# Performance work log

Measured on AMD Instinct MI355X. Metric: run time of the kernel, lower is better.

The kernel has to match this reference:

```python
import jax, jax.numpy as jnp
import numpy as np

B, V, FN, C = 8, 50000, 100000, 64


def setup_inputs() -> dict:
    key = jax.random.key(0)
    keys = iter(jax.random.split(key, 16))
    inp = {}
    inp["centers"] = jax.random.normal(next(keys), (B, 3, FN), jnp.float32)
    inp["verts"] = jax.random.normal(next(keys), (B, V, 3), jnp.float32)
    inp["faces"] = jax.random.randint(next(keys), (B, FN, 3), 0, V)

    def bn(p):
        inp[p + "g"] = jnp.ones((C,), jnp.float32)
        inp[p + "bt"] = jnp.zeros((C,), jnp.float32)
        inp[p + "m"] = jnp.zeros((C,), jnp.float32)
        inp[p + "v"] = jnp.ones((C,), jnp.float32)

    inp["cw1"] = jax.random.normal(next(keys), (C, 3), jnp.float32) * 0.1
    inp["cb1"] = jnp.zeros((C,), jnp.float32); bn("c1")
    inp["cw2"] = jax.random.normal(next(keys), (C, C), jnp.float32) * 0.1
    inp["cb2"] = jnp.zeros((C,), jnp.float32); bn("c2")
    inp["vw1"] = jax.random.normal(next(keys), (C, 6), jnp.float32) * 0.1
    inp["vb1"] = jnp.zeros((C,), jnp.float32); bn("v1")
    inp["vw2"] = jax.random.normal(next(keys), (C, C), jnp.float32) * 0.1
    inp["vb2"] = jnp.zeros((C,), jnp.float32); bn("v2")
    inp["sw"] = jax.random.normal(next(keys), (C, 2 * C), jnp.float32) * 0.1
    inp["sb"] = jnp.zeros((C,), jnp.float32); bn("s1")
    return inp


def _cbr(x, w, b, g, bt, m, v, eps=1e-5):
    # 1x1 Conv1d == pointwise GEMM over channel dim, then eval-mode BN, then ReLU
    y = jnp.einsum('bcf,oc->bof', x, w) + b[:, None]
    y = (y - m[:, None]) * (g[:, None] / jnp.sqrt(v[:, None] + eps)) + bt[:, None]
    return jax.nn.relu(y)


def _forward(faces, centers, verts,
             cw1, cb1, c1g, c1bt, c1m, c1v, cw2, cb2, c2g, c2bt, c2m, c2v,
             vw1, vb1, v1g, v1bt, v1m, v1v, vw2, vb2, v2g, v2bt, v2m, v2v,
             sw, sb, s1g, s1bt, s1m, s1v):
    Bb, Fn, _ = faces.shape
    # gather 3 corner vertices per face: [B, 3F, 3] -> [B, 9, F] (v0xyz, v1xyz, v2xyz)
    idx = faces.reshape(Bb, Fn * 3)
    corners = jnp.take_along_axis(verts, idx[:, :, None], axis=1)
    c9 = corners.reshape(Bb, Fn, 9).transpose(0, 2, 1)

    def vmlp(x):
        return _cbr(_cbr(x, vw1, vb1, v1g, v1bt, v1m, v1v), vw2, vb2, v2g, v2bt, v2m, v2v)

    vfeat = (vmlp(c9[:, :6])
             + vmlp(c9[:, 3:9])
             + vmlp(jnp.concatenate([c9[:, 6:9], c9[:, :3]], axis=1))) / 3.0
    cfeat = _cbr(_cbr(centers, cw1, cb1, c1g, c1bt, c1m, c1v), cw2, cb2, c2g, c2bt, c2m, c2v)
    return _cbr(jnp.concatenate([cfeat, vfeat], axis=1), sw, sb, s1g, s1bt, s1m, s1v)


def reference(centers, verts, faces,
              cw1, cb1, c1g, c1bt, c1m, c1v, cw2, cb2, c2g, c2bt, c2m, c2v,
              vw1, vb1, v1g, v1bt, v1m, v1v, vw2, vb2, v2g, v2bt, v2m, v2v,
              sw, sb, s1g, s1bt, s1m, s1v):
    return _forward(faces, centers, verts,
                    cw1, cb1, c1g, c1bt, c1m, c1v, cw2, cb2, c2g, c2bt, c2m, c2v,
                    vw1, vb1, v1g, v1bt, v1m, v1v, vw2, vb2, v2g, v2bt, v2m, v2v,
                    sw, sb, s1g, s1bt, s1m, s1v)
```

## Files before the change

kernel.cpp:

```cpp
#include <hip/hip_runtime.h>
#include <cstddef>
#include <cstdint>

#define FN_ 100000
#define V_  50000
#define B_  8
#define WPB   8
#define NBLK  3125

#define WS_SHS 49152

typedef _Float16 f16;
typedef f16   f16x8 __attribute__((ext_vector_type(8)));
typedef float f32x4 __attribute__((ext_vector_type(4)));

struct Ptrs { const void* p[33]; };

union Pk8 { f16 h[8]; uint4 u; };
union FragU { uint32_t u[4]; f16x8 v; };

__device__ __forceinline__ uint32_t pack2(float a, float b) {
  return __builtin_bit_cast(uint32_t, __builtin_amdgcn_cvt_pkrtz(a, b));
}
__device__ __forceinline__ uint32_t pack_relu2(float a, float b) {
  uint32_t r, x = pack2(a, b);
  asm("v_pk_max_f16 %0, %1, 0" : "=v"(r) : "v"(x));
  return r;
}

__global__ __launch_bounds__(1024) void sd_prep(Ptrs in, f16* __restrict__ wsW,
                                                float* __restrict__ shsG)
{
  const float* __restrict__ cw1 = (const float*)in.p[3];
  const float* __restrict__ cb1 = (const float*)in.p[4];
  const float* __restrict__ c1g = (const float*)in.p[5];
  const float* __restrict__ c1bt= (const float*)in.p[6];
  const float* __restrict__ c1m = (const float*)in.p[7];
  const float* __restrict__ c1v = (const float*)in.p[8];
  const float* __restrict__ cw2 = (const float*)in.p[9];
  const float* __restrict__ cb2 = (const float*)in.p[10];
  const float* __restrict__ c2g = (const float*)in.p[11];
  const float* __restrict__ c2bt= (const float*)in.p[12];
  const float* __restrict__ c2m = (const float*)in.p[13];
  const float* __restrict__ c2v = (const float*)in.p[14];
  const float* __restrict__ vw1 = (const float*)in.p[15];
  const float* __restrict__ vb1 = (const float*)in.p[16];
  const float* __restrict__ v1g = (const float*)in.p[17];
  const float* __restrict__ v1bt= (const float*)in.p[18];
  const float* __restrict__ v1m = (const float*)in.p[19];
  const float* __restrict__ v1v = (const float*)in.p[20];
  const float* __restrict__ vw2 = (const float*)in.p[21];
  const float* __restrict__ vb2 = (const float*)in.p[22];
  const float* __restrict__ v2g = (const float*)in.p[23];
  const float* __restrict__ v2bt= (const float*)in.p[24];
  const float* __restrict__ v2m = (const float*)in.p[25];
  const float* __restrict__ v2v = (const float*)in.p[26];
  const float* __restrict__ sw  = (const float*)in.p[27];
  const float* __restrict__ sb  = (const float*)in.p[28];
  const float* __restrict__ s1g = (const float*)in.p[29];
  const float* __restrict__ s1bt= (const float*)in.p[30];
  const float* __restrict__ s1m = (const float*)in.p[31];
  const float* __restrict__ s1v = (const float*)in.p[32];

  __shared__ float scsL[448];
  __shared__ float shfL[256];
  const int tid = threadIdx.x;

  if (tid < 448) {
    const float *g, *v, *bb, *m, *bt; int o; float mul = 1.f;
    if (tid < 64)       { o = tid;      g=c1g; v=c1v; bb=cb1; m=c1m; bt=c1bt; }
    else if (tid < 256) { o = tid & 63; g=v1g; v=v1v; bb=vb1; m=v1m; bt=v1bt; }
    else if (tid < 320) { o = tid-256;  g=c2g; v=c2v; bb=cb2; m=c2m; bt=c2bt; }
    else if (tid < 384) { o = tid-320;  g=v2g; v=v2v; bb=vb2; m=v2m; bt=v2bt; mul = 1.f/3.f; }
    else                { o = tid-384;  g=s1g; v=s1v; bb=sb;  m=s1m; bt=s1bt; }
    float s = g[o] * rsqrtf(v[o] + 1e-5f);
    float sh = ((bb[o] - m[o]) * s + bt[o]) * mul;
    scsL[tid] = s * mul;
    shsG[tid] = sh;
    if (tid < 256) shfL[tid] = sh;
  }
  __syncthreads();

  for (int u = tid; u < 3072; u += 1024) {
    const int t = u >> 6, l = u & 63, r15 = l & 15, g4 = l >> 4;
    Pk8 pk;
    if (t < 16) {
      const int wm = t >> 2, tr = t & 3, row = 64*wm + 16*tr + r15;
#pragma unroll
      for (int j = 0; j < 8; ++j) {
        const int k = 8*g4 + j; float val = 0.f;
        if (wm == 0) { if (k >= 9 && k < 12) val = cw1[row*3 + (k-9)]; }
        else if (k < 9) {
          const int e = wm - 1, o = row - 64*wm, c = (k - 3*e + 9) % 9;
          if (c < 6) val = vw1[o*6 + c];
        }
        pk.h[j] = (k == 12) ? (f16)shfL[row] : (f16)(val * scsL[row]);
      }
    } else if (t < 24) {
      const int tt = t-16, rt = tt >> 1, s = tt & 1, row = 16*rt + r15;
#pragma unroll
      for (int j = 0; j < 8; ++j) { const int k = 32*s + 8*g4 + j;
        pk.h[j] = (f16)(cw2[row*64 + k] * scsL[256+row]); }
    } else if (t < 32) {
      const int tt = t-24, rt = tt >> 1, s = tt & 1, row = 16*rt + r15;
#pragma unroll
      for (int j = 0; j < 8; ++j) { const int k = 32*s + 8*g4 + j;
        pk.h[j] = (f16)(vw2[row*64 + k] * scsL[320+row]); }
    } else {
      const int tt = t-32, rt = tt >> 2, s = tt & 3, row = 16*rt + r15;
#pragma unroll
      for (int j = 0; j < 8; ++j) { const int k = 32*s + 8*g4 + j;
        pk.h[j] = (f16)(sw[row*128 + k] * scsL[384+row]); }
    }
    *(uint4*)(wsW + (size_t)t*512 + l*8) = pk.u;
  }
}

__global__ __launch_bounds__(512, 4) void sd_main(const int* __restrict__ faces,
    const float* __restrict__ verts, const float* __restrict__ centers,
    const f16* __restrict__ wsW, const float* __restrict__ shsG,
    float* __restrict__ out)
{
  __shared__ f16  Wl[32 * 512];
  __shared__ f16  Ab[WPB][32 * 64];
  __shared__ float shsL[192];

  const int tid  = threadIdx.x;
  const int lane = tid & 63;
  const int r15  = lane & 15;
  const int g4   = lane >> 4;
  const int w    = __builtin_amdgcn_readfirstlane(tid >> 6);
  const int sw   = (r15 & 7) << 3;

  {
    const uint4* src = (const uint4*)wsW;
    uint4* dst = (uint4*)Wl;
#pragma unroll
    for (int i = 0; i < 4; ++i) dst[tid + i*512] = src[tid + i*512];
  }
  if (tid < 192) shsL[tid] = shsG[256 + tid];

  const int wt = blockIdx.x * WPB + w;
  const int by = wt / 3125;
  const int f0 = (wt - by * 3125) * 32;

  FragU xf[2];
#pragma unroll
  for (int c = 0; c < 2; ++c) {
    float vals[8] = {0.f,0.f,0.f,0.f,0.f,0.f,0.f,0.f};
    const int f = f0 + 16*c + r15;
    if (g4 == 0) {
      const size_t fb3 = ((size_t)by*FN_ + f)*3;
      const int i0 = faces[fb3], i1 = faces[fb3+1], i2 = faces[fb3+2];
      const float* q0 = verts + ((size_t)by*V_ + (size_t)i0)*3;
      const float* q1 = verts + ((size_t)by*V_ + (size_t)i1)*3;
      const float* q2 = verts + ((size_t)by*V_ + (size_t)i2)*3;
      vals[0]=q0[0]; vals[1]=q0[1]; vals[2]=q0[2];
      vals[3]=q1[0]; vals[4]=q1[1]; vals[5]=q1[2];
      vals[6]=q2[0]; vals[7]=q2[1];
    } else if (g4 == 1) {
      const size_t fb3 = ((size_t)by*FN_ + f)*3;
      const int i2 = faces[fb3+2];
      const float* q2 = verts + ((size_t)by*V_ + (size_t)i2)*3;
      vals[0]=q2[2];
      vals[1]=centers[((size_t)by*3+0)*FN_ + f];
      vals[2]=centers[((size_t)by*3+1)*FN_ + f];
      vals[3]=centers[((size_t)by*3+2)*FN_ + f];
      vals[4]=1.0f;
    }
#pragma unroll
    for (int m = 0; m < 4; ++m) xf[c].u[m] = pack2(vals[2*m], vals[2*m+1]);
  }
  __syncthreads();

  f16* ab = &Ab[w][0];

  float    vf[4][2][4];
  uint32_t cfp[4][2][2];

#pragma unroll
  for (int br = 0; br < 4; ++br) {
    f32x4 acc1[4][2];
#pragma unroll
    for (int t4 = 0; t4 < 4; ++t4) {
      const f16x8 a = *(const f16x8*)&Wl[(4*br + t4)*512 + lane*8];
#pragma unroll
      for (int c = 0; c < 2; ++c) {
        f32x4 z = {0.f,0.f,0.f,0.f};
        acc1[t4][c] = __builtin_amdgcn_mfma_f32_16x16x32_f16(a, xf[c].v, z, 0,0,0);
      }
    }
#pragma unroll
    for (int t4 = 0; t4 < 4; ++t4)
#pragma unroll
      for (int c = 0; c < 2; ++c) {
        uint2 pw;
        pw.x = pack_relu2(acc1[t4][c][0], acc1[t4][c][1]);
        pw.y = pack_relu2(acc1[t4][c][2], acc1[t4][c][3]);
        *(uint2*)&ab[(16*c + r15)*64 + ((16*t4 + 4*g4) ^ sw)] = pw;
      }

    f16x8 b2[2][2];
#pragma unroll
    for (int c = 0; c < 2; ++c)
#pragma unroll
      for (int s = 0; s < 2; ++s)
        b2[c][s] = *(const f16x8*)&ab[(16*c + r15)*64 + ((32*s + 8*g4) ^ sw)];

    const int wb = br ? 24 : 16;
    const int shb = br ? 64 : 0;
#pragma unroll
    for (int rt = 0; rt < 4; ++rt) {
      const f16x8 a0 = *(const f16x8*)&Wl[(wb + 2*rt    )*512 + lane*8];
      const f16x8 a1 = *(const f16x8*)&Wl[(wb + 2*rt + 1)*512 + lane*8];
      const f32x4 shv = *(const f32x4*)&shsL[shb + rt*16 + 4*g4];
#pragma unroll
      for (int c = 0; c < 2; ++c) {
        f32x4 acc = __builtin_amdgcn_mfma_f32_16x16x32_f16(a0, b2[c][0], shv, 0,0,0);
        acc = __builtin_amdgcn_mfma_f32_16x16x32_f16(a1, b2[c][1], acc, 0,0,0);
        if (br == 0) {
          cfp[rt][c][0] = pack_relu2(acc[0], acc[1]);
          cfp[rt][c][1] = pack_relu2(acc[2], acc[3]);
        } else if (br == 1) {
#pragma unroll
          for (int j = 0; j < 4; ++j) vf[rt][c][j] = fmaxf(acc[j], 0.f);
        } else {
#pragma unroll
          for (int j = 0; j < 4; ++j) vf[rt][c][j] += fmaxf(acc[j], 0.f);
        }
      }
    }
  }

  f32x4 acc3[4][2];
#pragma unroll
  for (int rt = 0; rt < 4; ++rt) {
    const f32x4 shv = *(const f32x4*)&shsL[128 + rt*16 + 4*g4];
    acc3[rt][0] = shv; acc3[rt][1] = shv;
  }

#pragma unroll
  for (int half = 0; half < 2; ++half) {
#pragma unroll
    for (int rt = 0; rt < 4; ++rt)
#pragma unroll
      for (int c = 0; c < 2; ++c) {
        uint2 pw;
        if (half == 0) { pw.x = cfp[rt][c][0]; pw.y = cfp[rt][c][1]; }
        else { pw.x = pack2(vf[rt][c][0], vf[rt][c][1]);
               pw.y = pack2(vf[rt][c][2], vf[rt][c][3]); }
        *(uint2*)&ab[(16*c + r15)*64 + ((16*rt + 4*g4) ^ sw)] = pw;
      }
#pragma unroll
    for (int s = 0; s < 2; ++s) {
      f16x8 b[2];
#pragma unroll
      for (int c = 0; c < 2; ++c)
        b[c] = *(const f16x8*)&ab[(16*c + r15)*64 + ((32*s + 8*g4) ^ sw)];
#pragma unroll
      for (int rt = 0; rt < 4; ++rt) {
        const f16x8 aS = *(const f16x8*)(wsW + (size_t)(32 + 4*rt + 2*half + s)*512 + lane*8);
        acc3[rt][0] = __builtin_amdgcn_mfma_f32_16x16x32_f16(aS, b[0], acc3[rt][0], 0,0,0);
        acc3[rt][1] = __builtin_amdgcn_mfma_f32_16x16x32_f16(aS, b[1], acc3[rt][1], 0,0,0);
      }
    }
  }

#pragma unroll
  for (int rt = 0; rt < 4; ++rt)
#pragma unroll
    for (int c = 0; c < 2; ++c) {
      const size_t base = ((size_t)(by*64 + rt*16 + 4*g4))*FN_ + (size_t)(f0 + 16*c + r15);
#pragma unroll
      for (int j = 0; j < 4; ++j)
        out[base + (size_t)j*FN_] = fmaxf(acc3[rt][c][j], 0.f);
    }
}

extern "C" void kernel_launch(void* const* d_in, const int* in_sizes, int n_in,
                              void* d_out, int out_size, void* d_ws, size_t ws_size,
                              hipStream_t stream) {
  (void)in_sizes; (void)n_in; (void)out_size; (void)ws_size;
  Ptrs p;
  for (int i = 0; i < 33; ++i) p.p[i] = d_in[i];
  f16*   wsW  = (f16*)d_ws;
  float* shsG = (float*)((char*)d_ws + WS_SHS);
  hipLaunchKernelGGL(sd_prep, dim3(1), dim3(1024), 0, stream, p, wsW, shsG);
  hipLaunchKernelGGL(sd_main, dim3(NBLK), dim3(512), 0, stream,
                     (const int*)d_in[2], (const float*)d_in[1], (const float*)d_in[0],
                     wsW, shsG, (float*)d_out);
}
```

Baseline: 89.05 us.

## Use 16x16x16 MFMA for first layer and keep weights in registers

The K=13 first-layer GEMM now uses the 16x16x16 f16 MFMA with 4-half fragments instead of a zero-padded K=32 MFMA. The packed weight workspace is rearranged so that layer-1 weights and the vertex second-layer weights are loaded straight from global memory into registers, and shared memory keeps only the center second-layer weights. This shrinks the per-block LDS weight copy from 32 KB to 8 KB and halves layer-1 MFMA work. The cost is higher register pressure, which could reduce occupancy or cause spills.

Measured after the change: 117.0 us. 1.31x slower.

```diff
diff --git a/kernel.cpp b/kernel.cpp
--- a/kernel.cpp
+++ b/kernel.cpp
@@ -8,16 +8,18 @@
 #define WPB   8
 #define NBLK  3125
 
-#define WS_SHS 49152
+#define WS_SHS_OFF 40960
 
 typedef _Float16 f16;
+typedef f16   f16x4 __attribute__((ext_vector_type(4)));
 typedef f16   f16x8 __attribute__((ext_vector_type(8)));
 typedef float f32x4 __attribute__((ext_vector_type(4)));
 
 struct Ptrs { const void* p[33]; };
 
+union Pk4h { f16 h[4]; uint2 u; };
 union Pk8 { f16 h[8]; uint4 u; };
-union FragU { uint32_t u[4]; f16x8 v; };
+union FragU4 { uint32_t u[2]; f16x4 v; };
 
 __device__ __forceinline__ uint32_t pack2(float a, float b) {
   return __builtin_bit_cast(uint32_t, __builtin_amdgcn_cvt_pkrtz(a, b));
@@ -81,38 +83,44 @@
   }
   __syncthreads();
 
-  for (int u = tid; u < 3072; u += 1024) {
-    const int t = u >> 6, l = u & 63, r15 = l & 15, g4 = l >> 4;
+  {
+    const int t = tid >> 6, l = tid & 63, r15l = l & 15, g4l = l >> 4;
+    const int row = 16*t + r15l;
+    const int wm = t >> 2;
+    Pk4h pk;
+#pragma unroll
+    for (int j = 0; j < 4; ++j) {
+      const int k = 4*g4l + j; float val = 0.f;
+      if (wm == 0) { if (k >= 9 && k < 12) val = cw1[row*3 + (k-9)]; }
+      else if (k < 9) {
+        const int e = wm - 1, o = row - 64*wm, c = (k - 3*e + 9) % 9;
+        if (c < 6) val = vw1[o*6 + c];
+      }
+      pk.h[j] = (k == 12) ? (f16)shfL[row] : (f16)(val * scsL[row]);
+    }
+    *(uint2*)((char*)wsW + t*512 + l*8) = pk.u;
+  }
+
+  for (int u = tid; u < 2560; u += 1024) {
+    const int t = u >> 6, l = u & 63, r15l = l & 15, g4l = l >> 4;
     Pk8 pk;
-    if (t < 16) {
-      const int wm = t >> 2, tr = t & 3, row = 64*wm + 16*tr + r15;
-#pragma unroll
-      for (int j = 0; j < 8; ++j) {
-        const int k = 8*g4 + j; float val = 0.f;
-        if (wm == 0) { if (k >= 9 && k < 12) val = cw1[row*3 + (k-9)]; }
-        else if (k < 9) {
-          const int e = wm - 1, o = row - 64*wm, c = (k - 3*e + 9) % 9;
-          if (c < 6) val = vw1[o*6 + c];
-        }
-        pk.h[j] = (k == 12) ? (f16)shfL[row] : (f16)(val * scsL[row]);
-      }
-    } else if (t < 24) {
-      const int tt = t-16, rt = tt >> 1, s = tt & 1, row = 16*rt + r15;
-#pragma unroll
-      for (int j = 0; j < 8; ++j) { const int k = 32*s + 8*g4 + j;
+    if (t < 8) {
+      const int rt = t >> 1, s = t & 1, row = 16*rt + r15l;
+#pragma unroll
+      for (int j = 0; j < 8; ++j) { const int k = 32*s + 8*g4l + j;
         pk.h[j] = (f16)(cw2[row*64 + k] * scsL[256+row]); }
-    } else if (t < 32) {
-      const int tt = t-24, rt = tt >> 1, s = tt & 1, row = 16*rt + r15;
-#pragma unroll
-      for (int j = 0; j < 8; ++j) { const int k = 32*s + 8*g4 + j;
+    } else if (t < 16) {
+      const int tt = t-8, rt = tt >> 1, s = tt & 1, row = 16*rt + r15l;
+#pragma unroll
+      for (int j = 0; j < 8; ++j) { const int k = 32*s + 8*g4l + j;
         pk.h[j] = (f16)(vw2[row*64 + k] * scsL[320+row]); }
     } else {
-      const int tt = t-32, rt = tt >> 2, s = tt & 3, row = 16*rt + r15;
-#pragma unroll
-      for (int j = 0; j < 8; ++j) { const int k = 32*s + 8*g4 + j;
+      const int tt = t-16, rt = tt >> 2, s4 = tt & 3, row = 16*rt + r15l;
+#pragma unroll
+      for (int j = 0; j < 8; ++j) { const int k = 32*s4 + 8*g4l + j;
         pk.h[j] = (f16)(sw[row*128 + k] * scsL[384+row]); }
     }
-    *(uint4*)(wsW + (size_t)t*512 + l*8) = pk.u;
+    *(uint4*)((char*)wsW + 8192 + t*1024 + l*16) = pk.u;
   }
 }
 
@@ -121,7 +129,7 @@
     const f16* __restrict__ wsW, const float* __restrict__ shsG,
     float* __restrict__ out)
 {
-  __shared__ f16  Wl[32 * 512];
+  __shared__ f16  Wl[8 * 512];
   __shared__ f16  Ab[WPB][32 * 64];
   __shared__ float shsL[192];
 
@@ -133,10 +141,8 @@
   const int sw   = (r15 & 7) << 3;
 
   {
-    const uint4* src = (const uint4*)wsW;
-    uint4* dst = (uint4*)Wl;
-#pragma unroll
-    for (int i = 0; i < 4; ++i) dst[tid + i*512] = src[tid + i*512];
+    const uint4* src = (const uint4*)((const char*)wsW + 8192);
+    ((uint4*)Wl)[tid] = src[tid];
   }
   if (tid < 192) shsL[tid] = shsG[256 + tid];
 
@@ -144,33 +150,45 @@
   const int by = wt / 3125;
   const int f0 = (wt - by * 3125) * 32;
 
-  FragU xf[2];
+  FragU4 xf[2];
 #pragma unroll
   for (int c = 0; c < 2; ++c) {
-    float vals[8] = {0.f,0.f,0.f,0.f,0.f,0.f,0.f,0.f};
+    float vals[4] = {0.f, 0.f, 0.f, 0.f};
     const int f = f0 + 16*c + r15;
+    const size_t fb3 = ((size_t)by*FN_ + f)*3;
     if (g4 == 0) {
-      const size_t fb3 = ((size_t)by*FN_ + f)*3;
-      const int i0 = faces[fb3], i1 = faces[fb3+1], i2 = faces[fb3+2];
+      const int i0 = faces[fb3], i1 = faces[fb3+1];
       const float* q0 = verts + ((size_t)by*V_ + (size_t)i0)*3;
       const float* q1 = verts + ((size_t)by*V_ + (size_t)i1)*3;
+      vals[0]=q0[0]; vals[1]=q0[1]; vals[2]=q0[2]; vals[3]=q1[0];
+    } else if (g4 == 1) {
+      const int i1 = faces[fb3+1], i2 = faces[fb3+2];
+      const float* q1 = verts + ((size_t)by*V_ + (size_t)i1)*3;
       const float* q2 = verts + ((size_t)by*V_ + (size_t)i2)*3;
-      vals[0]=q0[0]; vals[1]=q0[1]; vals[2]=q0[2];
-      vals[3]=q1[0]; vals[4]=q1[1]; vals[5]=q1[2];
-      vals[6]=q2[0]; vals[7]=q2[1];
-    } else if (g4 == 1) {
-      const size_t fb3 = ((size_t)by*FN_ + f)*3;
+      vals[0]=q1[1]; vals[1]=q1[2]; vals[2]=q2[0]; vals[3]=q2[1];
+    } else if (g4 == 2) {
       const int i2 = faces[fb3+2];
       const float* q2 = verts + ((size_t)by*V_ + (size_t)i2)*3;
       vals[0]=q2[2];
       vals[1]=centers[((size_t)by*3+0)*FN_ + f];
       vals[2]=centers[((size_t)by*3+1)*FN_ + f];
       vals[3]=centers[((size_t)by*3+2)*FN_ + f];
-      vals[4]=1.0f;
-    }
-#pragma unroll
-    for (int m = 0; m < 4; ++m) xf[c].u[m] = pack2(vals[2*m], vals[2*m+1]);
-  }
+    } else {
+      vals[0]=1.0f;
+    }
+    xf[c].u[0] = pack2(vals[0], vals[1]);
+    xf[c].u[1] = pack2(vals[2], vals[3]);
+  }
+
+  f16x4 l1a[16];
+#pragma unroll
+  for (int t = 0; t < 16; ++t)
+    l1a[t] = *(const f16x4*)((const char*)wsW + t*512 + lane*8);
+  f16x8 v2r[8];
+#pragma unroll
+  for (int i = 0; i < 8; ++i)
+    v2r[i] = *(const f16x8*)((const char*)wsW + 16384 + i*1024 + lane*16);
+
   __syncthreads();
 
   f16* ab = &Ab[w][0];
@@ -183,11 +201,11 @@
     f32x4 acc1[4][2];
 #pragma unroll
     for (int t4 = 0; t4 < 4; ++t4) {
-      const f16x8 a = *(const f16x8*)&Wl[(4*br + t4)*512 + lane*8];
+      const f16x4 a = l1a[4*br + t4];
 #pragma unroll
       for (int c = 0; c < 2; ++c) {
         f32x4 z = {0.f,0.f,0.f,0.f};
-        acc1[t4][c] = __builtin_amdgcn_mfma_f32_16x16x32_f16(a, xf[c].v, z, 0,0,0);
+        acc1[t4][c] = __builtin_amdgcn_mfma_f32_16x16x16f16(a, xf[c].v, z, 0,0,0);
       }
     }
 #pragma unroll
@@ -207,12 +225,11 @@
       for (int s = 0; s < 2; ++s)
         b2[c][s] = *(const f16x8*)&ab[(16*c + r15)*64 + ((32*s + 8*g4) ^ sw)];
 
-    const int wb = br ? 24 : 16;
     const int shb = br ? 64 : 0;
 #pragma unroll
     for (int rt = 0; rt < 4; ++rt) {
-      const f16x8 a0 = *(const f16x8*)&Wl[(wb + 2*rt    )*512 + lane*8];
-      const f16x8 a1 = *(const f16x8*)&Wl[(wb + 2*rt + 1)*512 + lane*8];
+      const f16x8 a0 = br ? v2r[2*rt]     : *(const f16x8*)&Wl[(2*rt    )*512 + lane*8];
+      const f16x8 a1 = br ? v2r[2*rt + 1] : *(const f16x8*)&Wl[(2*rt + 1)*512 + lane*8];
       const f32x4 shv = *(const f32x4*)&shsL[shb + rt*16 + 4*g4];
 #pragma unroll
       for (int c = 0; c < 2; ++c) {
@@ -259,7 +276,8 @@
         b[c] = *(const f16x8*)&ab[(16*c + r15)*64 + ((32*s + 8*g4) ^ sw)];
 #pragma unroll
       for (int rt = 0; rt < 4; ++rt) {
-        const f16x8 aS = *(const f16x8*)(wsW + (size_t)(32 + 4*rt + 2*half + s)*512 + lane*8);
+        const f16x8 aS = *(const f16x8*)((const char*)wsW + 24576
+                                         + (4*rt + 2*half + s)*1024 + lane*16);
         acc3[rt][0] = __builtin_amdgcn_mfma_f32_16x16x32_f16(aS, b[0], acc3[rt][0], 0,0,0);
         acc3[rt][1] = __builtin_amdgcn_mfma_f32_16x16x32_f16(aS, b[1], acc3[rt][1], 0,0,0);
       }
@@ -284,7 +302,7 @@
   Ptrs p;
   for (int i = 0; i < 33; ++i) p.p[i] = d_in[i];
   f16*   wsW  = (f16*)d_ws;
-  float* shsG = (float*)((char*)d_ws + WS_SHS);
+  float* shsG = (float*)((char*)d_ws + WS_SHS_OFF);
   hipLaunchKernelGGL(sd_prep, dim3(1), dim3(1024), 0, stream, p, wsW, shsG);
   hipLaunchKernelGGL(sd_main, dim3(NBLK), dim3(512), 0, stream,
                      (const int*)d_in[2], (const float*)d_in[1], (const float*)d_in[0],
```
